# Kernel tuning notes

Hardware: AMD Instinct MI355X
Metric: run time of the kernel (lower is better)

Reference implementation:

```python
import jax, jax.numpy as jnp
import numpy as np

B, S, D = 4, 2048, 1024
H = 16
HD = D // H  # 64


def setup_inputs() -> dict:
    key = jax.random.key(0)
    ks = jax.random.split(key, 5)
    s = 0.02
    return {
        "x": jax.random.normal(ks[0], (B, S, D), dtype=jnp.float32),
        "w_qkv": jax.random.normal(ks[1], (D, 3 * D), dtype=jnp.float32) * s,
        "b_qkv": jnp.zeros((3 * D,), dtype=jnp.float32),
        "w_out": jax.random.normal(ks[2], (D, D), dtype=jnp.float32) * s,
        "b_out": jnp.zeros((D,), dtype=jnp.float32),
    }


def reference(x, w_qkv, b_qkv, w_out, b_out):
    b, s, d = x.shape
    qkv = x @ w_qkv + b_qkv                              # [b,s,3d]
    qkv = qkv.reshape(b, s, 3, H, HD)
    q = qkv[:, :, 0].transpose(0, 2, 1, 3)               # [b,h,s,hd]
    k = qkv[:, :, 1].transpose(0, 2, 1, 3)
    v = qkv[:, :, 2].transpose(0, 2, 1, 3)
    scale = 1.0 / jnp.sqrt(jnp.asarray(HD, dtype=x.dtype))
    scores = jnp.einsum("bhqd,bhkd->bhqk", q, k) * scale  # [b,h,s,s]
    causal = jnp.tril(jnp.ones((s, s), dtype=bool))
    scores = jnp.where(causal[None, None], scores, jnp.asarray(-jnp.inf, dtype=x.dtype))
    probs = jax.nn.softmax(scores, axis=-1)
    out = jnp.einsum("bhqk,bhkd->bhqd", probs, v)        # [b,h,s,hd]
    out = out.transpose(0, 2, 1, 3).reshape(b, s, d)
    return out @ w_out + b_out
```

## Files before the change

kernel.cpp:

```cpp
#include <hip/hip_runtime.h>
#include <hip/hip_bf16.h>

typedef __bf16 bf16_t;
typedef __bf16 bf16x4 __attribute__((ext_vector_type(4)));
typedef __bf16 bf16x8 __attribute__((ext_vector_type(8)));
typedef float f32x4 __attribute__((ext_vector_type(4)));

#define Bb 4
#define Ss 2048
#define Dd 1024
#define Hh 16
#define HDd 64

#define QSC 0.1803368801111244f

__device__ __forceinline__ void gld16(const bf16_t* g, bf16_t* l) {
  __builtin_amdgcn_global_load_lds(
      (const __attribute__((address_space(1))) unsigned int*)g,
      (__attribute__((address_space(3))) unsigned int*)l, 16, 0, 0);
}

__global__ __launch_bounds__(256) void conv_to_bf16(
    const float* __restrict__ src, bf16_t* __restrict__ dst) {
  int i = (blockIdx.x * 256 + threadIdx.x) * 4;
  float4 v = *(const float4*)&src[i];
  bf16x4 o = {(bf16_t)v.x, (bf16_t)v.y, (bf16_t)v.z, (bf16_t)v.w};
  *(bf16x4*)&dst[i] = o;
}

__global__ __launch_bounds__(256) void transpose_conv(
    const float* __restrict__ in, bf16_t* __restrict__ out, int R, int C) {
  __shared__ bf16_t tile[32][33];
  int c0 = blockIdx.x * 32, r0 = blockIdx.y * 32;
  int tx = threadIdx.x, ty = threadIdx.y;
#pragma unroll
  for (int j = 0; j < 32; j += 8)
    tile[ty + j][tx] = (bf16_t)in[(size_t)(r0 + ty + j) * C + c0 + tx];
  __syncthreads();
#pragma unroll
  for (int j = 0; j < 32; j += 8)
    out[(size_t)(c0 + ty + j) * R + r0 + tx] = tile[tx][ty + j];
}

template <int MODE>
__global__ __launch_bounds__(512, 2) void gemm_8p(
    const bf16_t* __restrict__ A, const bf16_t* __restrict__ Bt,
    const float* __restrict__ bias, float* __restrict__ outf,
    bf16_t* __restrict__ out0, bf16_t* __restrict__ out1,
    bf16_t* __restrict__ out2, int M, int N, int K) {
  const int tid = threadIdx.x;
  const int lane = tid & 63;
  const int wave = tid >> 6;
  const int quad = lane >> 4;
  const int lr = lane & 15;
  const int wr = wave >> 1;
  const int wc = wave & 1;
  const int m0 = blockIdx.y * 256;
  const int n0 = blockIdx.x * 128;

  __shared__ __align__(16) bf16_t As[3][256 * 64];
  __shared__ __align__(16) bf16_t Bs[3][128 * 64];

  const f32x4 zero = {0.f, 0.f, 0.f, 0.f};
  f32x4 acc[4][4];
#pragma unroll
  for (int mi = 0; mi < 4; ++mi)
#pragma unroll
    for (int ni = 0; ni < 4; ++ni) acc[mi][ni] = zero;

  int ar[4], ac[4], br[2], bc[2];
#pragma unroll
  for (int i = 0; i < 4; ++i) {
    int c = tid + i * 512;
    ar[i] = c >> 3;
    ac[i] = ((c & 7) ^ (ar[i] & 7)) * 8;
  }
#pragma unroll
  for (int i = 0; i < 2; ++i) {
    int c = tid + i * 512;
    br[i] = c >> 3;
    bc[i] = ((c & 7) ^ (br[i] & 7)) * 8;
  }

  const int nk = K >> 6;

  auto stageA = [&](int t, int s) {
    const int ko = t << 6;
#pragma unroll
    for (int i = 0; i < 4; ++i)
      gld16(&A[(size_t)(m0 + ar[i]) * K + ko + ac[i]],
            &As[s][(tid + i * 512) * 8]);
  };
  auto stageB = [&](int t, int s) {
    const int ko = t << 6;
#pragma unroll
    for (int i = 0; i < 2; ++i)
      gld16(&Bt[(size_t)(n0 + br[i]) * K + ko + bc[i]],
            &Bs[s][(tid + i * 512) * 8]);
  };

  stageA(0, 0); stageB(0, 0);
  stageA(1, 1); stageB(1, 1);
  asm volatile("s_waitcnt vmcnt(6)" ::: "memory");
  __builtin_amdgcn_s_barrier();

  const int sx = lr & 7;
  const int arow = wr * 64 + lr;
  const int brow = wc * 64 + lr;

  int scur = 0;
  for (int t = 0; t < nk; ++t) {
    const bf16_t* as = As[scur];
    const bf16_t* bs = Bs[scur];
    int s2 = scur + 2;
    if (s2 >= 3) s2 -= 3;
    const bool pre = (t + 2 < nk);
#pragma unroll
    for (int ks = 0; ks < 2; ++ks) {
      bf16x8 af[4], bfr[4];
      const int cx = (((ks << 2) | quad) ^ sx) * 8;
#pragma unroll
      for (int mi = 0; mi < 4; ++mi)
        af[mi] = *(const bf16x8*)&as[(arow + mi * 16) * 64 + cx];
#pragma unroll
      for (int ni = 0; ni < 4; ++ni)
        bfr[ni] = *(const bf16x8*)&bs[(brow + ni * 16) * 64 + cx];
      if (ks == 0) {
        if (pre) stageA(t + 2, s2);
      } else {
        if (pre) stageB(t + 2, s2);
      }
      __builtin_amdgcn_s_barrier();
      asm volatile("s_waitcnt lgkmcnt(0)" ::: "memory");
      __builtin_amdgcn_sched_barrier(0);
      __builtin_amdgcn_s_setprio(1);
#pragma unroll
      for (int mi = 0; mi < 4; ++mi)
#pragma unroll
        for (int ni = 0; ni < 4; ++ni)
          acc[mi][ni] = __builtin_amdgcn_mfma_f32_16x16x32_bf16(
              af[mi], bfr[ni], acc[mi][ni], 0, 0, 0);
      __builtin_amdgcn_s_setprio(0);
      if (ks == 0) {
        __builtin_amdgcn_s_barrier();
      } else if (t + 1 < nk) {
        if (pre)
          asm volatile("s_waitcnt vmcnt(6)" ::: "memory");
        else
          asm volatile("s_waitcnt vmcnt(0)" ::: "memory");
        __builtin_amdgcn_s_barrier();
      }
    }
    scur = (scur == 2) ? 0 : scur + 1;
  }

#pragma unroll
  for (int mi = 0; mi < 4; ++mi) {
    const int mbase = m0 + wr * 64 + mi * 16 + quad * 4;
#pragma unroll
    for (int ni = 0; ni < 4; ++ni) {
      const int n = n0 + wc * 64 + ni * 16 + lr;
      const float bv = bias[n];
      if (MODE == 1) {
#pragma unroll
        for (int r = 0; r < 4; ++r)
          outf[(size_t)(mbase + r) * N + n] = acc[mi][ni][r] + bv;
      } else {
        const int which = n >> 10;
        const int h = (n >> 6) & 15;
        const int hd = n & 63;
        const int b = mbase >> 11;
        const int s = mbase & 2047;
        if (which == 2) {
          bf16x4 pk = {(bf16_t)(acc[mi][ni][0] + bv),
                       (bf16_t)(acc[mi][ni][1] + bv),
                       (bf16_t)(acc[mi][ni][2] + bv),
                       (bf16_t)(acc[mi][ni][3] + bv)};
          *(bf16x4*)&out2[(((size_t)(b * Hh + h)) * HDd + hd) * Ss + s] = pk;
        } else {
          bf16_t* dst = (which == 0) ? out0 : out1;
          const float sc = (which == 0) ? QSC : 1.0f;
#pragma unroll
          for (int r = 0; r < 4; ++r)
            dst[(((size_t)(b * Hh + h)) * Ss + s + r) * HDd + hd] =
                (bf16_t)((acc[mi][ni][r] + bv) * sc);
        }
      }
    }
  }
}

__global__ __launch_bounds__(256) void attn_kernel(
    const bf16_t* __restrict__ Qg, const bf16_t* __restrict__ Kg,
    const bf16_t* __restrict__ Vtg, bf16_t* __restrict__ Og) {
  const int tid = threadIdx.x;
  const int lane = tid & 63;
  const int wave = tid >> 6;
  const int quad = lane >> 4;
  const int lr = lane & 15;
  const int l7 = lr & 7;

  const int bid = blockIdx.x;
  const int xcd = bid & 7;
  const int j = bid >> 3;
  const int bh = xcd * 8 + (j >> 3);
  const int p = j & 7;
  const int b = bh >> 4;
  const int h = bh & 15;
  const int wq = wave * 32;

  const bf16_t* Qp = Qg + (size_t)bh * Ss * HDd;
  const bf16_t* Kp = Kg + (size_t)bh * Ss * HDd;
  const bf16_t* Vp = Vtg + (size_t)bh * HDd * Ss;

  __shared__ bf16_t Ks[2][64 * 64];
  __shared__ bf16_t Vts[2][64 * 64];
  __shared__ bf16_t Ps[4][32 * 64];

  bf16x8 kreg[2], vreg[2];
  const int r0 = tid >> 3;
  const int c0 = (tid & 7) * 8;
  const int swz = ((tid & 7) ^ ((tid >> 3) & 7)) * 8;

  const f32x4 zero = {0.f, 0.f, 0.f, 0.f};

#pragma unroll
  for (int i = 0; i < 2; ++i) {
    kreg[i] = *(const bf16x8*)&Kp[(size_t)(r0 + i * 32) * HDd + c0];
    vreg[i] = *(const bf16x8*)&Vp[(size_t)(r0 + i * 32) * Ss + c0];
  }

  int cur = 0;
  for (int half = 0; half < 2; ++half) {
    const int qt = half ? p : 15 - p;
    const int qbase = qt * 128;
    const int ktiles = qt * 2 + 2;

    bf16x8 bq[2][2];
#pragma unroll
    for (int qt2 = 0; qt2 < 2; ++qt2)
#pragma unroll
      for (int kk2 = 0; kk2 < 2; ++kk2)
        bq[qt2][kk2] = *(const bf16x8*)&Qp[(size_t)(qbase + wq + qt2 * 16 +
                                                    lr) *
                                               HDd +
                                           kk2 * 32 + quad * 8];

    f32x4 oacc[4][2];
#pragma unroll
    for (int dt = 0; dt < 4; ++dt)
#pragma unroll
      for (int qt2 = 0; qt2 < 2; ++qt2) oacc[dt][qt2] = zero;
    float l_run[2] = {0.f, 0.f};

    for (int kt = 0; kt < ktiles; ++kt) {
      const int kbase = kt * 64;

#pragma unroll
      for (int i = 0; i < 2; ++i) {
        *(bf16x8*)&Ks[cur][(r0 + i * 32) * 64 + swz] = kreg[i];
        *(bf16x8*)&Vts[cur][(r0 + i * 32) * 64 + swz] = vreg[i];
      }
      __syncthreads();

      const int nkb = (kt + 1 < ktiles) ? kbase + 64 : 0;
#pragma unroll
      for (int i = 0; i < 2; ++i) {
        kreg[i] = *(const bf16x8*)&Kp[(size_t)(nkb + r0 + i * 32) * HDd + c0];
        vreg[i] = *(const bf16x8*)&Vp[(size_t)(r0 + i * 32) * Ss + nkb + c0];
      }

      f32x4 sacc[4][2];
#pragma unroll
      for (int kt4 = 0; kt4 < 4; ++kt4)
#pragma unroll
        for (int qt2 = 0; qt2 < 2; ++qt2) sacc[kt4][qt2] = zero;
#pragma unroll
      for (int kk2 = 0; kk2 < 2; ++kk2) {
        const int rsl = (((kk2 << 2) | quad) ^ l7) * 8;
        bf16x8 ak[4];
#pragma unroll
        for (int kt4 = 0; kt4 < 4; ++kt4)
          ak[kt4] = *(const bf16x8*)&Ks[cur][(kt4 * 16 + lr) * 64 + rsl];
#pragma unroll
        for (int kt4 = 0; kt4 < 4; ++kt4)
#pragma unroll
          for (int qt2 = 0; qt2 < 2; ++qt2)
            sacc[kt4][qt2] = __builtin_amdgcn_mfma_f32_16x16x32_bf16(
                ak[kt4], bq[qt2][kk2], sacc[kt4][qt2], 0, 0, 0);
      }

      const bool edge = (kt >= 2 * qt);
#pragma unroll
      for (int kt4 = 0; kt4 < 4; ++kt4)
#pragma unroll
        for (int qt2 = 0; qt2 < 2; ++qt2)
#pragma unroll
          for (int r = 0; r < 4; ++r) {
            float s = sacc[kt4][qt2][r];
            if (edge) {
              const int qg = qbase + wq + qt2 * 16 + lr;
              const int kg = kbase + kt4 * 16 + quad * 4 + r;
              if (kg > qg) s = -1e30f;
            }
            const float pv = __builtin_amdgcn_exp2f(s);
            sacc[kt4][qt2][r] = pv;
            l_run[qt2] += pv;
          }

#pragma unroll
      for (int kt4 = 0; kt4 < 4; ++kt4) {
        const int psl = ((kt4 * 2 + (quad >> 1)) ^ l7) * 8 + (quad & 1) * 4;
#pragma unroll
        for (int qt2 = 0; qt2 < 2; ++qt2) {
          bf16x4 pk = {(bf16_t)sacc[kt4][qt2][0], (bf16_t)sacc[kt4][qt2][1],
                       (bf16_t)sacc[kt4][qt2][2], (bf16_t)sacc[kt4][qt2][3]};
          *(bf16x4*)&Ps[wave][(qt2 * 16 + lr) * 64 + psl] = pk;
        }
      }

#pragma unroll
      for (int kk2 = 0; kk2 < 2; ++kk2) {
        const int rsl = (((kk2 << 2) | quad) ^ l7) * 8;
        bf16x8 av[4], bp[2];
#pragma unroll
        for (int dt = 0; dt < 4; ++dt)
          av[dt] = *(const bf16x8*)&Vts[cur][(dt * 16 + lr) * 64 + rsl];
#pragma unroll
        for (int qt2 = 0; qt2 < 2; ++qt2)
          bp[qt2] = *(const bf16x8*)&Ps[wave][(qt2 * 16 + lr) * 64 + rsl];
#pragma unroll
        for (int dt = 0; dt < 4; ++dt)
#pragma unroll
          for (int qt2 = 0; qt2 < 2; ++qt2)
            oacc[dt][qt2] = __builtin_amdgcn_mfma_f32_16x16x32_bf16(
                av[dt], bp[qt2], oacc[dt][qt2], 0, 0, 0);
      }
      cur ^= 1;
    }

#pragma unroll
    for (int qt2 = 0; qt2 < 2; ++qt2) {
      l_run[qt2] += __shfl_xor(l_run[qt2], 16, 64);
      l_run[qt2] += __shfl_xor(l_run[qt2], 32, 64);
    }

#pragma unroll
    for (int qt2 = 0; qt2 < 2; ++qt2) {
      const float inv = 1.f / l_run[qt2];
      const int qg = qbase + wq + qt2 * 16 + lr;
#pragma unroll
      for (int dt = 0; dt < 4; ++dt) {
        bf16x4 ov = {(bf16_t)(oacc[dt][qt2][0] * inv),
                     (bf16_t)(oacc[dt][qt2][1] * inv),
                     (bf16_t)(oacc[dt][qt2][2] * inv),
                     (bf16_t)(oacc[dt][qt2][3] * inv)};
        *(bf16x4*)&Og[((size_t)b * Ss + qg) * Dd + h * HDd + dt * 16 +
                      quad * 4] = ov;
      }
    }
  }
}

extern "C" void kernel_launch(void* const* d_in, const int* in_sizes, int n_in,
                              void* d_out, int out_size, void* d_ws,
                              size_t ws_size, hipStream_t stream) {
  const float* x = (const float*)d_in[0];
  const float* w_qkv = (const float*)d_in[1];
  const float* b_qkv = (const float*)d_in[2];
  const float* w_out = (const float*)d_in[3];
  const float* b_out = (const float*)d_in[4];
  float* out = (float*)d_out;

  bf16_t* Kb = (bf16_t*)d_ws;
  bf16_t* Vt = Kb + (size_t)Bb * Hh * Ss * HDd;
  bf16_t* slot3 = Vt + (size_t)Bb * Hh * Ss * HDd;
  bf16_t* Wt1 = slot3;
  bf16_t* Ob = slot3;
  bf16_t* Wt2 = Kb;
  bf16_t* Qb = (bf16_t*)d_out;
  bf16_t* Xc = (bf16_t*)d_out + (size_t)8192 * 1024;

  conv_to_bf16<<<8192, 256, 0, stream>>>(x, Xc);
  transpose_conv<<<dim3(96, 32), dim3(32, 8), 0, stream>>>(w_qkv, Wt1, 1024,
                                                           3072);

  gemm_8p<0><<<dim3(24, 32), 512, 0, stream>>>(
      Xc, Wt1, b_qkv, nullptr, Qb, Kb, Vt, 8192, 3072, 1024);

  attn_kernel<<<dim3(512), 256, 0, stream>>>(Qb, Kb, Vt, Ob);

  transpose_conv<<<dim3(32, 32), dim3(32, 8), 0, stream>>>(w_out, Wt2, 1024,
                                                           1024);

  gemm_8p<1><<<dim3(8, 32), 512, 0, stream>>>(
      Ob, Wt2, b_out, out, nullptr, nullptr, nullptr, 8192, 1024, 1024);
}
```

Before: 257.5 us.

## Fuse input prep kernels and compute softmax row sums via MFMA

Merges the fp32-to-bf16 conversion of x and the w_qkv transpose-convert into one launch that dispatches on block index, removing a kernel launch and its gap. In the attention kernel, the per-lane scalar accumulation of exp values plus the cross-lane shuffle reduction is replaced by an extra MFMA that multiplies the bf16 P tile by a ones vector, so the row sums come out of the matrix unit. This adds two MFMAs per k-chunk and sums the bf16-rounded probabilities rather than the fp32 ones. That slightly changes the normaliser but makes it consistent with what P·V actually uses.

Measured after the change: 263.4 us. 1.02x slower.

```diff
diff --git a/kernel.cpp b/kernel.cpp
--- a/kernel.cpp
+++ b/kernel.cpp
@@ -20,12 +20,29 @@
       (__attribute__((address_space(3))) unsigned int*)l, 16, 0, 0);
 }
 
-__global__ __launch_bounds__(256) void conv_to_bf16(
-    const float* __restrict__ src, bf16_t* __restrict__ dst) {
-  int i = (blockIdx.x * 256 + threadIdx.x) * 4;
-  float4 v = *(const float4*)&src[i];
-  bf16x4 o = {(bf16_t)v.x, (bf16_t)v.y, (bf16_t)v.z, (bf16_t)v.w};
-  *(bf16x4*)&dst[i] = o;
+__global__ __launch_bounds__(256) void prep(
+    const float* __restrict__ x, bf16_t* __restrict__ Xc,
+    const float* __restrict__ w_qkv, bf16_t* __restrict__ Wt1) {
+  __shared__ bf16_t tile[32][33];
+  const int b = blockIdx.x;
+  const int tid = threadIdx.x;
+  if (b < 8192) {
+    int i = (b * 256 + tid) * 4;
+    float4 v = *(const float4*)&x[i];
+    bf16x4 o = {(bf16_t)v.x, (bf16_t)v.y, (bf16_t)v.z, (bf16_t)v.w};
+    *(bf16x4*)&Xc[i] = o;
+  } else {
+    const int id = b - 8192;
+    const int c0 = (id % 96) * 32, r0 = (id / 96) * 32;
+    const int tx = tid & 31, ty = tid >> 5;
+#pragma unroll
+    for (int j = 0; j < 32; j += 8)
+      tile[ty + j][tx] = (bf16_t)w_qkv[(size_t)(r0 + ty + j) * 3072 + c0 + tx];
+    __syncthreads();
+#pragma unroll
+    for (int j = 0; j < 32; j += 8)
+      Wt1[(size_t)(c0 + ty + j) * 1024 + r0 + tx] = tile[tx][ty + j];
+  }
 }
 
 __global__ __launch_bounds__(256) void transpose_conv(
@@ -223,6 +240,9 @@
   const int swz = ((tid & 7) ^ ((tid >> 3) & 7)) * 8;
 
   const f32x4 zero = {0.f, 0.f, 0.f, 0.f};
+  bf16x8 ones1;
+#pragma unroll
+  for (int i = 0; i < 8; ++i) ones1[i] = (bf16_t)1.0f;
 
 #pragma unroll
   for (int i = 0; i < 2; ++i) {
@@ -251,7 +271,9 @@
     for (int dt = 0; dt < 4; ++dt)
 #pragma unroll
       for (int qt2 = 0; qt2 < 2; ++qt2) oacc[dt][qt2] = zero;
-    float l_run[2] = {0.f, 0.f};
+    f32x4 lacc[2];
+    lacc[0] = zero;
+    lacc[1] = zero;
 
     for (int kt = 0; kt < ktiles; ++kt) {
       const int kbase = kt * 64;
@@ -303,9 +325,7 @@
               const int kg = kbase + kt4 * 16 + quad * 4 + r;
               if (kg > qg) s = -1e30f;
             }
-            const float pv = __builtin_amdgcn_exp2f(s);
-            sacc[kt4][qt2][r] = pv;
-            l_run[qt2] += pv;
+            sacc[kt4][qt2][r] = __builtin_amdgcn_exp2f(s);
           }
 
 #pragma unroll
@@ -335,19 +355,17 @@
           for (int qt2 = 0; qt2 < 2; ++qt2)
             oacc[dt][qt2] = __builtin_amdgcn_mfma_f32_16x16x32_bf16(
                 av[dt], bp[qt2], oacc[dt][qt2], 0, 0, 0);
+#pragma unroll
+        for (int qt2 = 0; qt2 < 2; ++qt2)
+          lacc[qt2] = __builtin_amdgcn_mfma_f32_16x16x32_bf16(
+              ones1, bp[qt2], lacc[qt2], 0, 0, 0);
       }
       cur ^= 1;
     }
 
 #pragma unroll
     for (int qt2 = 0; qt2 < 2; ++qt2) {
-      l_run[qt2] += __shfl_xor(l_run[qt2], 16, 64);
-      l_run[qt2] += __shfl_xor(l_run[qt2], 32, 64);
-    }
-
-#pragma unroll
-    for (int qt2 = 0; qt2 < 2; ++qt2) {
-      const float inv = 1.f / l_run[qt2];
+      const float inv = 1.f / lacc[qt2][0];
       const int qg = qbase + wq + qt2 * 16 + lr;
 #pragma unroll
       for (int dt = 0; dt < 4; ++dt) {
@@ -381,9 +399,7 @@
   bf16_t* Qb = (bf16_t*)d_out;
   bf16_t* Xc = (bf16_t*)d_out + (size_t)8192 * 1024;
 
-  conv_to_bf16<<<8192, 256, 0, stream>>>(x, Xc);
-  transpose_conv<<<dim3(96, 32), dim3(32, 8), 0, stream>>>(w_qkv, Wt1, 1024,
-                                                           3072);
+  prep<<<11264, 256, 0, stream>>>(x, Xc, w_qkv, Wt1);
 
   gemm_8p<0><<<dim3(24, 32), 512, 0, stream>>>(
       Xc, Wt1, b_qkv, nullptr, Qb, Kb, Vt, 8192, 3072, 1024);
```
